# Kernel tuning notes

Measured on AMD Instinct MI355X. Metric: run time of the kernel, lower is better.

The kernel has to match this reference:

```python
import jax, jax.numpy as jnp
import numpy as np


def setup_inputs() -> dict:
    key = jax.random.key(0)
    ks = jax.random.split(key, 7)
    B, D, K, L = 32768, 256, 8, 4
    s = 1.0 / np.sqrt(D)
    return {
        "x": jax.random.normal(ks[0], (B, D), jnp.float32),
        "gate_W": jax.random.normal(ks[1], (D, K), jnp.float32) * s,
        "gate_b": jax.random.normal(ks[2], (K,), jnp.float32) * s,
        "block_W": jax.random.normal(ks[3], (L, K, D, D), jnp.float32) * s,
        "block_b": jax.random.normal(ks[4], (L, K, D), jnp.float32) * s,
        "out_W": jax.random.normal(ks[5], (K, D, D), jnp.float32) * s,
        "out_b": jax.random.normal(ks[6], (K, D), jnp.float32) * s,
    }


def _moie_block(x, alpha, W, b):
    # x: (B, in), alpha: (B, K), W: (K, in, out), b: (K, out)
    z = jnp.einsum('bi,kio->bko', x, W) + b[None]        # (B, K, out)
    return jnp.einsum('bk,bko->bo', alpha, z)            # alpha-weighted sum over experts


def reference(x, gate_W, gate_b, block_W, block_b, out_W, out_b):
    # standard gating: softmax(Linear(x)); same alpha reused at every layer
    alpha = jax.nn.softmax(x @ gate_W + gate_b, axis=-1)  # (B, K)
    h = x
    num_layers = block_W.shape[0]
    for i in range(num_layers):
        h = jax.nn.relu(_moie_block(h, alpha, block_W[i], block_b[i]))
    # output block, no activation
    return _moie_block(h, alpha, out_W, out_b)
```

## Files before the change

kernel.cpp:

```cpp
#include <hip/hip_runtime.h>
#include <hip/hip_bf16.h>

typedef __attribute__((ext_vector_type(8))) _Float16 h8v;
typedef __attribute__((ext_vector_type(4))) float f4v;

__device__ __forceinline__ ushort f16bits(float f) {
    _Float16 h = (_Float16)f;
    return __builtin_bit_cast(unsigned short, h);
}

__global__ __launch_bounds__(256) void gate_kernel(
    const float* __restrict__ x, const float* __restrict__ gW,
    const float* __restrict__ gb, float* __restrict__ alpha)
{
    int lane = threadIdx.x & 63;
    int wave = threadIdx.x >> 6;
    int row = blockIdx.x * 4 + wave;
    float4 xv = *(const float4*)(x + (size_t)row * 256 + lane * 4);
    const float* xp = (const float*)&xv;
    float p[8];
#pragma unroll
    for (int k = 0; k < 8; ++k) p[k] = 0.f;
#pragma unroll
    for (int j = 0; j < 4; ++j) {
        float xs = xp[j];
        const float* wr = gW + (lane * 4 + j) * 8;
#pragma unroll
        for (int k = 0; k < 8; ++k) p[k] = fmaf(xs, wr[k], p[k]);
    }
#pragma unroll
    for (int off = 32; off > 0; off >>= 1) {
#pragma unroll
        for (int k = 0; k < 8; ++k) p[k] += __shfl_xor(p[k], off);
    }
    float m = -1e30f;
#pragma unroll
    for (int k = 0; k < 8; ++k) { p[k] += gb[k]; m = fmaxf(m, p[k]); }
    float s = 0.f;
#pragma unroll
    for (int k = 0; k < 8; ++k) { p[k] = expf(p[k] - m); s += p[k]; }
    if (lane < 8) alpha[(size_t)row * 8 + lane] = p[lane] / s;
}

__global__ __launch_bounds__(256) void prep_weights(
    const float* __restrict__ blockW, const float* __restrict__ outW,
    ushort* __restrict__ Wg)
{
    const int m = blockIdx.x >> 3;
    const int g = blockIdx.x & 7;
    const float* src = (m < 32) ? (blockW + (size_t)m * 65536)
                                : (outW + (size_t)(m - 32) * 65536);
    const int o = threadIdx.x;
    uint pk[16];
#pragma unroll
    for (int kp = 0; kp < 16; ++kp) {
        float f0 = src[(size_t)(g * 32 + 2 * kp) * 256 + o];
        float f1 = src[(size_t)(g * 32 + 2 * kp + 1) * 256 + o];
        pk[kp] = (uint)f16bits(f0) | ((uint)f16bits(f1) << 16);
    }
    size_t base = (size_t)(m >> 3) * 524288 + (size_t)((m & 7) * 8 + g) * 8192
                + (size_t)o * 32;
    *(uint4*)(Wg + base)      = make_uint4(pk[0],  pk[1],  pk[2],  pk[3]);
    *(uint4*)(Wg + base + 8)  = make_uint4(pk[4],  pk[5],  pk[6],  pk[7]);
    *(uint4*)(Wg + base + 16) = make_uint4(pk[8],  pk[9],  pk[10], pk[11]);
    *(uint4*)(Wg + base + 24) = make_uint4(pk[12], pk[13], pk[14], pk[15]);
}

template<bool RELU>
__global__ __launch_bounds__(256, 2) void moie_gemm(
    const float* __restrict__ Hin, float* __restrict__ Hout,
    const ushort* __restrict__ Wg,
    const float* __restrict__ bias, const float* __restrict__ alpha)
{
    __shared__ __align__(16) ushort Ah[64 * 256];

    const int tid  = threadIdx.x;
    const int lane = tid & 63;
    const int wid  = tid >> 6;
    const int m0   = blockIdx.x * 64;
    const int wcol0 = wid * 64;
    const int kgl = lane >> 4;
    const int fr  = lane & 15;

    float areg[4][8];
#pragma unroll
    for (int im = 0; im < 4; ++im) {
        const float4* ap = (const float4*)(alpha + (size_t)(m0 + im * 16 + fr) * 8);
        float4 a0 = ap[0], a1 = ap[1];
        areg[im][0] = a0.x; areg[im][1] = a0.y; areg[im][2] = a0.z; areg[im][3] = a0.w;
        areg[im][4] = a1.x; areg[im][5] = a1.y; areg[im][6] = a1.z; areg[im][7] = a1.w;
    }

    {
        const int r0  = tid >> 6;
        const int kk  = (tid & 63) * 4;
        const int kg  = kk >> 3;
        const int klo = kk & 7;
#pragma unroll
        for (int p = 0; p < 16; ++p) {
            int row = p * 4 + r0;
            float4 v = *(const float4*)(Hin + (size_t)(m0 + row) * 256 + kk);
            uint2 pkv;
            pkv.x = (uint)f16bits(v.x) | ((uint)f16bits(v.y) << 16);
            pkv.y = (uint)f16bits(v.z) | ((uint)f16bits(v.w) << 16);
            *(uint2*)&Ah[row * 256 + (kg ^ (row & 7)) * 8 + klo] = pkv;
        }
    }
    __syncthreads();

    const ushort* Wslice = Wg + (size_t)wcol0 * 32 + (size_t)(fr * 4 + kgl) * 8;

    f4v acc[4][4];
#pragma unroll
    for (int a = 0; a < 4; ++a)
#pragma unroll
        for (int b = 0; b < 4; ++b) acc[a][b] = (f4v){0.f, 0.f, 0.f, 0.f};

    h8v bfs[2][4];
#pragma unroll
    for (int in = 0; in < 4; ++in) {
        bfs[0][in] = *(const h8v*)(Wslice + (size_t)0 * 8192 + in * 512);
        bfs[1][in] = *(const h8v*)(Wslice + (size_t)8 * 8192 + in * 512);
    }

    h8v afc[4];

#pragma unroll 1
    for (int ki = 0; ki < 8; ++ki) {
        const int kg0 = ki * 4;
#pragma unroll
        for (int im = 0; im < 4; ++im) {
            int row = im * 16 + fr;
            afc[im] = *(const h8v*)&Ah[row * 256 + ((kg0 + kgl) ^ (row & 7)) * 8];
        }
#pragma unroll
        for (int e = 0; e < 8; ++e) {
            const int set = e & 1;
            h8v as[4];
#pragma unroll
            for (int im = 0; im < 4; ++im) {
                _Float16 ah = (_Float16)areg[im][e];
                as[im] = afc[im] * ah;
            }
            __builtin_amdgcn_s_setprio(1);
#pragma unroll
            for (int im = 0; im < 4; ++im)
#pragma unroll
                for (int in = 0; in < 4; ++in)
                    acc[im][in] = __builtin_amdgcn_mfma_f32_16x16x32_f16(
                        as[im], bfs[set][in], acc[im][in], 0, 0, 0);
            __builtin_amdgcn_s_setprio(0);
            int ne, nki;
            if (e < 6) { ne = e + 2; nki = ki; }
            else       { ne = e - 6; nki = ki + 1; }
            if (nki > 7) { nki = 7; ne = 7; }
            const ushort* tp = Wslice + (size_t)(ne * 8 + nki) * 8192;
#pragma unroll
            for (int in = 0; in < 4; ++in)
                bfs[set][in] = *(const h8v*)(tp + in * 512);
        }
    }

    float bv[4][8];
#pragma unroll
    for (int in = 0; in < 4; ++in) {
        int col = wcol0 + in * 16 + fr;
#pragma unroll
        for (int k = 0; k < 8; ++k) bv[in][k] = bias[k * 256 + col];
    }
#pragma unroll
    for (int im = 0; im < 4; ++im) {
#pragma unroll
        for (int j = 0; j < 4; ++j) {
            int row = m0 + im * 16 + kgl * 4 + j;
            const float4* ap = (const float4*)(alpha + (size_t)row * 8);
            float4 a0 = ap[0], a1 = ap[1];
            float a8[8] = {a0.x, a0.y, a0.z, a0.w, a1.x, a1.y, a1.z, a1.w};
#pragma unroll
            for (int in = 0; in < 4; ++in) {
                int col = wcol0 + in * 16 + fr;
                float be = 0.f;
#pragma unroll
                for (int k = 0; k < 8; ++k) be = fmaf(a8[k], bv[in][k], be);
                float v = acc[im][in][j] + be;
                if (RELU) v = fmaxf(v, 0.f);
                Hout[(size_t)row * 256 + col] = v;
            }
        }
    }
}

extern "C" void kernel_launch(void* const* d_in, const int* in_sizes, int n_in,
                              void* d_out, int out_size, void* d_ws, size_t ws_size,
                              hipStream_t stream)
{
    const float* x      = (const float*)d_in[0];
    const float* gW     = (const float*)d_in[1];
    const float* gb     = (const float*)d_in[2];
    const float* blockW = (const float*)d_in[3];
    const float* blockB = (const float*)d_in[4];
    const float* outW   = (const float*)d_in[5];
    const float* outB   = (const float*)d_in[6];
    float* out = (float*)d_out;

    char* ws = (char*)d_ws;
    float*  alpha = (float*)ws;
    ushort* Wg    = (ushort*)(ws + (1 << 20));

    prep_weights<<<320, 256, 0, stream>>>(blockW, outW, Wg);
    gate_kernel<<<8192, 256, 0, stream>>>(x, gW, gb, alpha);

    const size_t WL = (size_t)524288;
    moie_gemm<true ><<<512, 256, 0, stream>>>(x,   out, Wg,          blockB,            alpha);
    moie_gemm<true ><<<512, 256, 0, stream>>>(out, out, Wg + 1 * WL, blockB + 1 * 2048, alpha);
    moie_gemm<true ><<<512, 256, 0, stream>>>(out, out, Wg + 2 * WL, blockB + 2 * 2048, alpha);
    moie_gemm<true ><<<512, 256, 0, stream>>>(out, out, Wg + 3 * WL, blockB + 3 * 2048, alpha);
    moie_gemm<false><<<512, 256, 0, stream>>>(out, out, Wg + 4 * WL, outB,              alpha);
}
```

Baseline: 357.6 us.

## Store intermediate activations as fp16 and enlarge GEMM tile to 128 rows

Hidden activations between layers are now kept in an fp16 workspace buffer, so the intermediate read and write traffic is halved. Only the output layer writes fp32. Each GEMM block now covers 128 rows with 16 waves in a 4x4 arrangement, so four row-waves share the same weight fragments, and the weight prefetch moves from double-buffer depth 2 to one step ahead. Alpha is converted to fp16 once at the start. The trade-offs are extra fp16 rounding of activations, half as many blocks (one per CU), and a shorter prefetch distance.

```diff
diff --git a/kernel.cpp b/kernel.cpp
--- a/kernel.cpp
+++ b/kernel.cpp
@@ -66,29 +66,35 @@
     *(uint4*)(Wg + base + 24) = make_uint4(pk[12], pk[13], pk[14], pk[15]);
 }
 
-template<bool RELU>
-__global__ __launch_bounds__(256, 2) void moie_gemm(
-    const float* __restrict__ Hin, float* __restrict__ Hout,
-    const ushort* __restrict__ Wg,
-    const float* __restrict__ bias, const float* __restrict__ alpha)
-{
-    __shared__ __align__(16) ushort Ah[64 * 256];
+template<int MODE>
+__global__ __launch_bounds__(1024, 4) void moie_gemm(
+    const void* __restrict__ HinV, ushort* __restrict__ Hout16,
+    float* __restrict__ HoutF,
+    const ushort* __restrict__ Wg, const float* __restrict__ bias,
+    const float* __restrict__ alpha)
+{
+    __shared__ __align__(16) ushort Ah[128 * 256];
 
     const int tid  = threadIdx.x;
     const int lane = tid & 63;
     const int wid  = tid >> 6;
-    const int m0   = blockIdx.x * 64;
-    const int wcol0 = wid * 64;
+    const int wr   = wid >> 2;
+    const int wc   = wid & 3;
+    const int m0   = blockIdx.x * 128;
+    const int wrow0 = wr * 32;
+    const int wcol0 = wc * 64;
     const int kgl = lane >> 4;
     const int fr  = lane & 15;
 
-    float areg[4][8];
-#pragma unroll
-    for (int im = 0; im < 4; ++im) {
-        const float4* ap = (const float4*)(alpha + (size_t)(m0 + im * 16 + fr) * 8);
+    _Float16 ah[2][8];
+#pragma unroll
+    for (int im = 0; im < 2; ++im) {
+        const float4* ap = (const float4*)(alpha + (size_t)(m0 + wrow0 + im * 16 + fr) * 8);
         float4 a0 = ap[0], a1 = ap[1];
-        areg[im][0] = a0.x; areg[im][1] = a0.y; areg[im][2] = a0.z; areg[im][3] = a0.w;
-        areg[im][4] = a1.x; areg[im][5] = a1.y; areg[im][6] = a1.z; areg[im][7] = a1.w;
+        ah[im][0] = (_Float16)a0.x; ah[im][1] = (_Float16)a0.y;
+        ah[im][2] = (_Float16)a0.z; ah[im][3] = (_Float16)a0.w;
+        ah[im][4] = (_Float16)a1.x; ah[im][5] = (_Float16)a1.y;
+        ah[im][6] = (_Float16)a1.z; ah[im][7] = (_Float16)a1.w;
     }
 
     {
@@ -97,67 +103,70 @@
         const int kg  = kk >> 3;
         const int klo = kk & 7;
 #pragma unroll
-        for (int p = 0; p < 16; ++p) {
-            int row = p * 4 + r0;
-            float4 v = *(const float4*)(Hin + (size_t)(m0 + row) * 256 + kk);
-            uint2 pkv;
-            pkv.x = (uint)f16bits(v.x) | ((uint)f16bits(v.y) << 16);
-            pkv.y = (uint)f16bits(v.z) | ((uint)f16bits(v.w) << 16);
-            *(uint2*)&Ah[row * 256 + (kg ^ (row & 7)) * 8 + klo] = pkv;
+        for (int p = 0; p < 8; ++p) {
+            int row = p * 16 + r0;
+            uint2 pk;
+            if (MODE == 0) {
+                const float* Hf = (const float*)HinV;
+                float4 v = *(const float4*)(Hf + (size_t)(m0 + row) * 256 + kk);
+                pk.x = (uint)f16bits(v.x) | ((uint)f16bits(v.y) << 16);
+                pk.y = (uint)f16bits(v.z) | ((uint)f16bits(v.w) << 16);
+            } else {
+                const ushort* Hh = (const ushort*)HinV;
+                pk = *(const uint2*)(Hh + (size_t)(m0 + row) * 256 + kk);
+            }
+            *(uint2*)&Ah[row * 256 + (kg ^ (row & 7)) * 8 + klo] = pk;
         }
     }
     __syncthreads();
 
-    const ushort* Wslice = Wg + (size_t)wcol0 * 32 + (size_t)(fr * 4 + kgl) * 8;
-
-    f4v acc[4][4];
-#pragma unroll
-    for (int a = 0; a < 4; ++a)
+    const ushort* Wslice = Wg + (size_t)(wcol0 + fr) * 32 + kgl * 8;
+
+    f4v acc[2][4];
+#pragma unroll
+    for (int a = 0; a < 2; ++a)
 #pragma unroll
         for (int b = 0; b < 4; ++b) acc[a][b] = (f4v){0.f, 0.f, 0.f, 0.f};
 
-    h8v bfs[2][4];
-#pragma unroll
-    for (int in = 0; in < 4; ++in) {
-        bfs[0][in] = *(const h8v*)(Wslice + (size_t)0 * 8192 + in * 512);
-        bfs[1][in] = *(const h8v*)(Wslice + (size_t)8 * 8192 + in * 512);
-    }
-
-    h8v afc[4];
+    h8v bcur[4], bnxt[4];
+#pragma unroll
+    for (int in = 0; in < 4; ++in)
+        bcur[in] = *(const h8v*)(Wslice + in * 512);
 
 #pragma unroll 1
     for (int ki = 0; ki < 8; ++ki) {
+        h8v afc[2];
         const int kg0 = ki * 4;
 #pragma unroll
-        for (int im = 0; im < 4; ++im) {
-            int row = im * 16 + fr;
+        for (int im = 0; im < 2; ++im) {
+            int row = wrow0 + im * 16 + fr;
             afc[im] = *(const h8v*)&Ah[row * 256 + ((kg0 + kgl) ^ (row & 7)) * 8];
         }
 #pragma unroll
         for (int e = 0; e < 8; ++e) {
-            const int set = e & 1;
-            h8v as[4];
-#pragma unroll
-            for (int im = 0; im < 4; ++im) {
-                _Float16 ah = (_Float16)areg[im][e];
-                as[im] = afc[im] * ah;
-            }
+            const int nt_e  = (e < 7) ? (e + 1) : 0;
+            const int nt_ki_static = (e < 7) ? 0 : 1;
+            int nki = ki + nt_ki_static;
+            if (nki > 7) nki = 7;
+            const ushort* tp = Wslice + (size_t)(nt_e * 8 + nki) * 8192;
+#pragma unroll
+            for (int in = 0; in < 4; ++in)
+                bnxt[in] = *(const h8v*)(tp + in * 512);
+            h8v as[2];
+#pragma unroll
+            for (int im = 0; im < 2; ++im)
+                as[im] = afc[im] * ah[im][e];
             __builtin_amdgcn_s_setprio(1);
 #pragma unroll
-            for (int im = 0; im < 4; ++im)
+            for (int im = 0; im < 2; ++im)
 #pragma unroll
                 for (int in = 0; in < 4; ++in)
                     acc[im][in] = __builtin_amdgcn_mfma_f32_16x16x32_f16(
-                        as[im], bfs[set][in], acc[im][in], 0, 0, 0);
+                        as[im], bcur[in], acc[im][in], 0, 0, 0);
             __builtin_amdgcn_s_setprio(0);
-            int ne, nki;
-            if (e < 6) { ne = e + 2; nki = ki; }
-            else       { ne = e - 6; nki = ki + 1; }
-            if (nki > 7) { nki = 7; ne = 7; }
-            const ushort* tp = Wslice + (size_t)(ne * 8 + nki) * 8192;
 #pragma unroll
             for (int in = 0; in < 4; ++in)
-                bfs[set][in] = *(const h8v*)(tp + in * 512);
+                bcur[in] = bnxt[in];
         }
     }
 
@@ -169,10 +178,10 @@
         for (int k = 0; k < 8; ++k) bv[in][k] = bias[k * 256 + col];
     }
 #pragma unroll
-    for (int im = 0; im < 4; ++im) {
+    for (int im = 0; im < 2; ++im) {
 #pragma unroll
         for (int j = 0; j < 4; ++j) {
-            int row = m0 + im * 16 + kgl * 4 + j;
+            int row = m0 + wrow0 + im * 16 + kgl * 4 + j;
             const float4* ap = (const float4*)(alpha + (size_t)row * 8);
             float4 a0 = ap[0], a1 = ap[1];
             float a8[8] = {a0.x, a0.y, a0.z, a0.w, a1.x, a1.y, a1.z, a1.w};
@@ -183,8 +192,11 @@
 #pragma unroll
                 for (int k = 0; k < 8; ++k) be = fmaf(a8[k], bv[in][k], be);
                 float v = acc[im][in][j] + be;
-                if (RELU) v = fmaxf(v, 0.f);
-                Hout[(size_t)row * 256 + col] = v;
+                if (MODE == 2) {
+                    HoutF[(size_t)row * 256 + col] = v;
+                } else {
+                    Hout16[(size_t)row * 256 + col] = f16bits(fmaxf(v, 0.f));
+                }
             }
         }
     }
@@ -206,14 +218,15 @@
     char* ws = (char*)d_ws;
     float*  alpha = (float*)ws;
     ushort* Wg    = (ushort*)(ws + (1 << 20));
+    ushort* H16   = (ushort*)(ws + (8 << 20));
 
     prep_weights<<<320, 256, 0, stream>>>(blockW, outW, Wg);
     gate_kernel<<<8192, 256, 0, stream>>>(x, gW, gb, alpha);
 
     const size_t WL = (size_t)524288;
-    moie_gemm<true ><<<512, 256, 0, stream>>>(x,   out, Wg,          blockB,            alpha);
-    moie_gemm<true ><<<512, 256, 0, stream>>>(out, out, Wg + 1 * WL, blockB + 1 * 2048, alpha);
-    moie_gemm<true ><<<512, 256, 0, stream>>>(out, out, Wg + 2 * WL, blockB + 2 * 2048, alpha);
-    moie_gemm<true ><<<512, 256, 0, stream>>>(out, out, Wg + 3 * WL, blockB + 3 * 2048, alpha);
-    moie_gemm<false><<<512, 256, 0, stream>>>(out, out, Wg + 4 * WL, outB,              alpha);
-}
+    moie_gemm<0><<<256, 1024, 0, stream>>>(x,   H16, nullptr, Wg,          blockB,            alpha);
+    moie_gemm<1><<<256, 1024, 0, stream>>>(H16, H16, nullptr, Wg + 1 * WL, blockB + 1 * 2048, alpha);
+    moie_gemm<1><<<256, 1024, 0, stream>>>(H16, H16, nullptr, Wg + 2 * WL, blockB + 2 * 2048, alpha);
+    moie_gemm<1><<<256, 1024, 0, stream>>>(H16, H16, nullptr, Wg + 3 * WL, blockB + 3 * 2048, alpha);
+    moie_gemm<2><<<256, 1024, 0, stream>>>(H16, nullptr, out, Wg + 4 * WL, outB,              alpha);
+}
```

After: 924.2 us. +158.4%, slower.
